# Optimization experiments

Measured on AMD Instinct MI355X. Metric: run time of the kernel, lower is better.

Reference implementation:

```python
import jax, jax.numpy as jnp
import numpy as np

# dims (see shape_source)
N = 100000          # num_ent
E = 400000          # num edges
B = 2048            # batch of (sub, rel) queries
INIT_DIM = 100
UFD = 100           # user_fe_dim
ENT_DIM = INIT_DIM + 3 * UFD   # feature_method='concat' -> 400
H = 2               # attention heads
D = 64              # per-head dim
GCN = H * D         # gcn_dim = embed_dim = 128 (gcn_layer == 1)
NUM_REL = 50
NR2 = 2 * NUM_REL


def setup_inputs() -> dict:
    key = jax.random.key(0)
    ks = jax.random.split(key, 17)
    inp = {}
    # constructor / forward int tensors
    inp["edge_index"] = jax.random.randint(ks[0], (2, E), 0, N, dtype=jnp.int32)
    inp["edge_type"] = jax.random.randint(ks[1], (E,), 0, NR2, dtype=jnp.int32)
    inp["edge_type_p"] = jax.random.randint(ks[2], (E,), 0, NR2, dtype=jnp.int32)
    inp["ent_feature"] = jax.random.randint(ks[3], (N, 3), 0, 3, dtype=jnp.int32)
    inp["sub"] = jax.random.randint(ks[4], (B,), 0, N, dtype=jnp.int32)
    inp["rel"] = jax.random.randint(ks[5], (B,), 0, NR2, dtype=jnp.int32)
    inp["relp"] = jax.random.randint(ks[6], (B,), 0, NR2, dtype=jnp.int32)
    # learned parameters
    s = 0.02
    inp["id_embed"] = jax.random.normal(ks[7], (N, INIT_DIM), jnp.float32) * s
    inp["gender_tab"] = jax.random.normal(ks[8], (3, UFD), jnp.float32) * s
    inp["age_tab"] = jax.random.normal(ks[9], (9, UFD), jnp.float32) * s
    inp["level_tab"] = jax.random.normal(ks[10], (11, UFD), jnp.float32) * s
    inp["init_rel"] = jax.random.normal(ks[11], (NR2, ENT_DIM), jnp.float32) * s
    inp["W"] = jax.random.normal(ks[12], (ENT_DIM, H * D), jnp.float32) * 0.05
    inp["Wr"] = jax.random.normal(ks[13], (ENT_DIM, H * D), jnp.float32) * 0.05
    inp["att_src"] = jax.random.normal(ks[14], (H, D), jnp.float32) * 0.05
    inp["att_dst"] = jax.random.normal(ks[15], (H, D), jnp.float32) * 0.05
    inp["Wrel"] = jax.random.normal(ks[16], (ENT_DIM, GCN), jnp.float32) * 0.05
    return inp


def _segment_softmax(logits, seg, num_segments):
    # logits: [E, H], seg: [E] destination node ids
    m = jax.ops.segment_max(logits, seg, num_segments=num_segments)
    ex = jnp.exp(logits - m[seg])
    den = jax.ops.segment_sum(ex, seg, num_segments=num_segments)
    return ex / (den[seg] + 1e-16)


def _rghat_conv(x, rel_emb, edge_index, edge_type, W, Wr, att_src, att_dst, Wrel):
    # relational multi-head graph attention (RGHATConv)
    n = x.shape[0]
    h = (x @ W).reshape(n, H, D)                       # [N,H,D] projected nodes
    r_proj = (rel_emb @ Wr).reshape(-1, H, D)          # [R,H,D]
    src, dst = edge_index[0], edge_index[1]
    msg = h[src] + r_proj[edge_type]                   # [E,H,D] edge messages
    logits = jax.nn.leaky_relu(
        jnp.sum(msg * att_src, axis=-1) + jnp.sum(h[dst] * att_dst, axis=-1),
        negative_slope=0.2,
    )                                                  # [E,H]
    alpha = _segment_softmax(logits, dst, n)           # per-destination softmax
    out = jax.ops.segment_sum(alpha[..., None] * msg, dst, num_segments=n)
    out = jnp.tanh(out.reshape(n, H * D))              # [N,GCN]
    r_out = rel_emb @ Wrel                             # [R,GCN]
    return out, r_out


def reference(edge_index, edge_type, edge_type_p, ent_feature, sub, rel, relp,
              id_embed, gender_tab, age_tab, level_tab, init_rel,
              W, Wr, att_src, att_dst, Wrel):
    # feature_method == 'concat': gather per-node feature embeddings and concat
    x1 = gender_tab[ent_feature[:, 0]]
    x2 = age_tab[ent_feature[:, 1]]
    x3 = level_tab[ent_feature[:, 2]]
    init_embed = jnp.concatenate([id_embed, x1, x2, x3], axis=1)  # [N, ENT_DIM]
    # single conv layer (gcn_layer == 1); dropouts are identity in eval
    x, r = _rghat_conv(init_embed, init_rel, edge_index, edge_type,
                       W, Wr, att_src, att_dst, Wrel)
    sub_emb = x[sub]                                   # index_select gather
    # add_parent_rel == False -> r returned whole (relp unused)
    return (sub_emb, r, x)
```

## Files before the change

### kernel.cpp

```cpp
#include <hip/hip_runtime.h>
#include <hip/hip_bf16.h>
#include <hip/hip_fp16.h>

#define N_NODES 100000
#define E_EDGES 400000
#define B_SUB 2048
#define INIT_DIM 100
#define UFD 100
#define ENT_DIM 400
#define GCN 128
#define NR2 100
#define KPAD 416
#define NCH 13
#define CAP 64

typedef __attribute__((ext_vector_type(8))) short shortx8;
typedef __attribute__((ext_vector_type(4))) float floatx4;

#define OUT_R_OFF ((long)B_SUB * GCN)
#define OUT_X_OFF ((long)(B_SUB + NR2) * GCN)

__device__ __forceinline__ unsigned short f2b(float f) {
    unsigned u = __float_as_uint(f);
    u += 0x7fffu + ((u >> 16) & 1u);
    return (unsigned short)(u >> 16);
}
__device__ __forceinline__ unsigned pk2(float x, float y) {
    return (unsigned)f2b(x) | ((unsigned)f2b(y) << 16);
}
__device__ __forceinline__ float blo(unsigned u) { return __uint_as_float(u << 16); }
__device__ __forceinline__ float bhi(unsigned u) { return __uint_as_float(u & 0xFFFF0000u); }

__global__ void wt_kernel(const float* __restrict__ W, unsigned short* __restrict__ Wt,
                          int* __restrict__ cursor) {
    int idx = blockIdx.x * 256 + threadIdx.x;
    if (idx < GCN * KPAD) {
        int n = idx & 127, k = idx >> 7;
        unsigned short o = 0;
        if (k < ENT_DIM) o = f2b(W[(long)k * GCN + n]);
        Wt[(long)n * KPAD + k] = o;
    }
    if (idx < N_NODES) cursor[idx] = 0;
}

__global__ void rel_kernel(const float* __restrict__ init_rel, const float* __restrict__ Wr,
                           const float* __restrict__ Wrel, const float* __restrict__ att_src,
                           unsigned* __restrict__ rp_b, float* __restrict__ rproj_att,
                           float* __restrict__ out_r) {
    int rel = blockIdx.x;
    int tx = threadIdx.x;
    __shared__ float rl[ENT_DIM];
    __shared__ float accbuf[128];
    for (int k = tx; k < ENT_DIM; k += 128) rl[k] = init_rel[(long)rel * ENT_DIM + k];
    __syncthreads();
    float acc1 = 0.f, acc2 = 0.f;
    for (int k = 0; k < ENT_DIM; ++k) {
        float v = rl[k];
        acc1 += v * Wr[(long)k * GCN + tx];
        acc2 += v * Wrel[(long)k * GCN + tx];
    }
    out_r[rel * GCN + tx] = acc2;
    accbuf[tx] = acc1;
    int head = tx >> 6, d = tx & 63;
    float v = acc1 * att_src[head * 64 + d];
    for (int off = 32; off > 0; off >>= 1) v += __shfl_down(v, off, 64);
    if (d == 0) rproj_att[rel * 2 + head] = v;
    __syncthreads();
    if (tx < 64) rp_b[rel * 64 + tx] = pk2(accbuf[tx], accbuf[tx + 64]);
}

__device__ __forceinline__ float4 load_seg(const float* __restrict__ id_embed,
                                           const float* __restrict__ gtab,
                                           const float* __restrict__ atab,
                                           const float* __restrict__ ltab,
                                           int n, int f0, int f1, int f2, int kg) {
    if (kg < 100)      return *(const float4*)&id_embed[(long)n * INIT_DIM + kg];
    else if (kg < 200) return *(const float4*)&gtab[f0 * UFD + kg - 100];
    else if (kg < 300) return *(const float4*)&atab[f1 * UFD + kg - 200];
    else if (kg < 400) return *(const float4*)&ltab[f2 * UFD + kg - 300];
    return make_float4(0.f, 0.f, 0.f, 0.f);
}

__global__ __launch_bounds__(256) void hgemm_kernel(
        const float* __restrict__ id_embed, const float* __restrict__ gtab,
        const float* __restrict__ atab, const float* __restrict__ ltab,
        const int* __restrict__ ent_feature, const unsigned short* __restrict__ Wt,
        const float* __restrict__ att_src, const float* __restrict__ att_dst,
        unsigned* __restrict__ h_b, float* __restrict__ hsrc_att, float* __restrict__ hdst_att) {
    __shared__ __align__(16) unsigned short As[64 * 40];
    __shared__ __align__(16) unsigned short Bs[128 * 40];
    __shared__ float attS[128], attD[128];
    int t = threadIdx.x;
    if (t < 128) { attS[t] = att_src[t]; attD[t] = att_dst[t]; }
    int n0 = blockIdx.x * 64;
    int row = t >> 2, seg = t & 3;
    int n = n0 + row;
    bool okn = n < N_NODES;
    int f0 = 0, f1 = 0, f2 = 0;
    if (okn) {
        f0 = ent_feature[n * 3];
        f1 = ent_feature[n * 3 + 1];
        f2 = ent_feature[n * 3 + 2];
    }
    int w = t >> 6, lane = t & 63, quad = lane >> 4, l16 = lane & 15;
    int nB0 = t >> 2,          k00 = (t & 3) * 8;
    int nB1 = (t + 256) >> 2,  k01 = (t & 3) * 8;

    floatx4 acc[8];
#pragma unroll
    for (int c = 0; c < 8; ++c) acc[c] = (floatx4){0.f, 0.f, 0.f, 0.f};

    float4 va = make_float4(0.f, 0.f, 0.f, 0.f), vb = va;
    if (okn) {
        va = load_seg(id_embed, gtab, atab, ltab, n, f0, f1, f2, seg * 8);
        vb = load_seg(id_embed, gtab, atab, ltab, n, f0, f1, f2, seg * 8 + 4);
    }
    shortx8 pb0 = *(const shortx8*)&Wt[(long)nB0 * KPAD + k00];
    shortx8 pb1 = *(const shortx8*)&Wt[(long)nB1 * KPAD + k01];

    for (int ch = 0; ch < NCH; ++ch) {
        uint4 u;
        u.x = pk2(va.x, va.y); u.y = pk2(va.z, va.w);
        u.z = pk2(vb.x, vb.y); u.w = pk2(vb.z, vb.w);
        __syncthreads();
        *(uint4*)&As[row * 40 + seg * 8] = u;
        *(shortx8*)&Bs[nB0 * 40 + k00] = pb0;
        *(shortx8*)&Bs[nB1 * 40 + k01] = pb1;
        if (ch + 1 < NCH) {
            int kg = (ch + 1) * 32 + seg * 8;
            if (okn) {
                va = load_seg(id_embed, gtab, atab, ltab, n, f0, f1, f2, kg);
                vb = load_seg(id_embed, gtab, atab, ltab, n, f0, f1, f2, kg + 4);
            }
            pb0 = *(const shortx8*)&Wt[(long)nB0 * KPAD + (ch + 1) * 32 + k00];
            pb1 = *(const shortx8*)&Wt[(long)nB1 * KPAD + (ch + 1) * 32 + k01];
        }
        __syncthreads();
        shortx8 a = *(shortx8*)&As[(w * 16 + l16) * 40 + quad * 8];
#pragma unroll
        for (int c = 0; c < 8; ++c) {
            shortx8 b = *(shortx8*)&Bs[(c * 16 + l16) * 40 + quad * 8];
            acc[c] = __builtin_amdgcn_mfma_f32_16x16x32_bf16(a, b, acc[c], 0, 0, 0);
        }
    }
    int baseRow = n0 + w * 16 + quad * 4;
#pragma unroll
    for (int i = 0; i < 4; ++i) {
        int node = baseRow + i;
        bool ok = node < N_NODES;
#pragma unroll
        for (int c = 0; c < 4; ++c)
            if (ok) h_b[(long)node * 64 + c * 16 + l16] = pk2(acc[c][i], acc[c + 4][i]);
        float s0 = 0.f, s1 = 0.f, d0 = 0.f, d1 = 0.f;
#pragma unroll
        for (int c = 0; c < 8; ++c) {
            float v = acc[c][i];
            float as_ = attS[c * 16 + l16], ad_ = attD[c * 16 + l16];
            if (c < 4) { s0 += v * as_; d0 += v * ad_; }
            else       { s1 += v * as_; d1 += v * ad_; }
        }
#pragma unroll
        for (int m = 1; m < 16; m <<= 1) {
            s0 += __shfl_xor(s0, m, 64);
            s1 += __shfl_xor(s1, m, 64);
            d0 += __shfl_xor(d0, m, 64);
            d1 += __shfl_xor(d1, m, 64);
        }
        if (ok && l16 == 0) {
            hsrc_att[node * 2] = s0; hsrc_att[node * 2 + 1] = s1;
            hdst_att[node * 2] = d0; hdst_att[node * 2 + 1] = d1;
        }
    }
}

__global__ void fill_kernel(const int* __restrict__ edge_index, const int* __restrict__ edge_type,
                            int* __restrict__ cursor,
                            const float2* __restrict__ hsrc2, const float2* __restrict__ rpa2,
                            const float2* __restrict__ hdst2,
                            uint2* __restrict__ ebuf) {
    int e = blockIdx.x * blockDim.x + threadIdx.x;
    if (e >= E_EDGES) return;
    int src = edge_index[e];
    int dst = edge_index[E_EDGES + e];
    int et = edge_type[e];
    float2 hs = hsrc2[src];
    float2 ra = rpa2[et];
    float2 hd = hdst2[dst];
    float x0 = hs.x + ra.x + hd.x;
    float x1 = hs.y + ra.y + hd.y;
    x0 = x0 > 0.f ? x0 : 0.2f * x0;
    x1 = x1 > 0.f ? x1 : 0.2f * x1;
    __half2 hh = __floats2half2_rn(__expf(x0), __expf(x1));
    union { __half2 h; unsigned u; } cv; cv.h = hh;
    int pos = atomicAdd(&cursor[dst], 1);
    if (pos < CAP)
        ebuf[(long)dst * CAP + pos] = make_uint2(((unsigned)et << 17) | (unsigned)src, cv.u);
}

__global__ __launch_bounds__(256) void agg_kernel(
        const int* __restrict__ cursor, const uint2* __restrict__ ebuf,
        const unsigned* __restrict__ h_b, const unsigned* __restrict__ rp_b,
        float* __restrict__ out_x) {
    int w = threadIdx.x >> 6, l = threadIdx.x & 63;
    int dst = blockIdx.x * 4 + w;
    int cnt = cursor[dst];
    if (cnt > CAP) cnt = CAP;
    const uint2* base = ebuf + (long)dst * CAP;
    float acc0 = 0.f, acc1 = 0.f, den0 = 0.f, den1 = 0.f;
    int j = 0;
    for (; j + 3 < cnt; j += 4) {
        uint2 v0 = base[j], v1 = base[j + 1], v2 = base[j + 2], v3 = base[j + 3];
        union { __half2 h; unsigned u; } c0, c1, c2, c3;
        c0.u = v0.y; c1.u = v1.y; c2.u = v2.y; c3.u = v3.y;
        float2 e0 = __half22float2(c0.h), e1 = __half22float2(c1.h);
        float2 e2 = __half22float2(c2.h), e3 = __half22float2(c3.h);
        unsigned hb0 = h_b[(long)(v0.x & 0x1FFFF) * 64 + l];
        unsigned hb1 = h_b[(long)(v1.x & 0x1FFFF) * 64 + l];
        unsigned hb2 = h_b[(long)(v2.x & 0x1FFFF) * 64 + l];
        unsigned hb3 = h_b[(long)(v3.x & 0x1FFFF) * 64 + l];
        unsigned rb0 = rp_b[(v0.x >> 17) * 64 + l];
        unsigned rb1 = rp_b[(v1.x >> 17) * 64 + l];
        unsigned rb2 = rp_b[(v2.x >> 17) * 64 + l];
        unsigned rb3 = rp_b[(v3.x >> 17) * 64 + l];
        acc0 += e0.x * (blo(hb0) + blo(rb0)) + e1.x * (blo(hb1) + blo(rb1))
              + e2.x * (blo(hb2) + blo(rb2)) + e3.x * (blo(hb3) + blo(rb3));
        acc1 += e0.y * (bhi(hb0) + bhi(rb0)) + e1.y * (bhi(hb1) + bhi(rb1))
              + e2.y * (bhi(hb2) + bhi(rb2)) + e3.y * (bhi(hb3) + bhi(rb3));
        den0 += e0.x + e1.x + e2.x + e3.x;
        den1 += e0.y + e1.y + e2.y + e3.y;
    }
    for (; j < cnt; ++j) {
        uint2 v0 = base[j];
        union { __half2 h; unsigned u; } c0; c0.u = v0.y;
        float2 e0 = __half22float2(c0.h);
        unsigned hb = h_b[(long)(v0.x & 0x1FFFF) * 64 + l];
        unsigned rb = rp_b[(v0.x >> 17) * 64 + l];
        acc0 += e0.x * (blo(hb) + blo(rb));
        acc1 += e0.y * (bhi(hb) + bhi(rb));
        den0 += e0.x;
        den1 += e0.y;
    }
    float i0 = 1.0f / (den0 + 1e-16f), i1 = 1.0f / (den1 + 1e-16f);
    out_x[(long)dst * GCN + l] = tanhf(acc0 * i0);
    out_x[(long)dst * GCN + 64 + l] = tanhf(acc1 * i1);
}

__global__ void gather_kernel(const int* __restrict__ sub, const float* __restrict__ out_x,
                              float* __restrict__ out_sub) {
    int idx = blockIdx.x * blockDim.x + threadIdx.x;
    if (idx >= B_SUB * GCN) return;
    int b = idx >> 7, d = idx & 127;
    out_sub[idx] = out_x[(long)sub[b] * GCN + d];
}

extern "C" void kernel_launch(void* const* d_in, const int* in_sizes, int n_in,
                              void* d_out, int out_size, void* d_ws, size_t ws_size,
                              hipStream_t stream) {
    const int* edge_index = (const int*)d_in[0];
    const int* edge_type  = (const int*)d_in[1];
    const int* ent_feature = (const int*)d_in[3];
    const int* sub = (const int*)d_in[4];
    const float* id_embed = (const float*)d_in[7];
    const float* gtab = (const float*)d_in[8];
    const float* atab = (const float*)d_in[9];
    const float* ltab = (const float*)d_in[10];
    const float* init_rel = (const float*)d_in[11];
    const float* W = (const float*)d_in[12];
    const float* Wr = (const float*)d_in[13];
    const float* att_src = (const float*)d_in[14];
    const float* att_dst = (const float*)d_in[15];
    const float* Wrel = (const float*)d_in[16];

    char* ws = (char*)d_ws;
    unsigned* h_b = (unsigned*)ws;                          ws += (long)N_NODES * 64 * 4;
    unsigned* rp_b = (unsigned*)ws;                         ws += (long)NR2 * 64 * 4;
    float* rproj_att = (float*)ws;                          ws += NR2 * 2 * 4;
    float* hsrc_att = (float*)ws;                           ws += (long)N_NODES * 2 * 4;
    float* hdst_att = (float*)ws;                           ws += (long)N_NODES * 2 * 4;
    unsigned short* Wt = (unsigned short*)ws;               ws += (long)GCN * KPAD * 2;
    int* cursor = (int*)ws;                                 ws += (long)N_NODES * 4;
    uint2* ebuf = (uint2*)ws;                               ws += (long)N_NODES * CAP * 8;

    float* out = (float*)d_out;
    float* out_sub = out;
    float* out_r = out + OUT_R_OFF;
    float* out_x = out + OUT_X_OFF;

    const int NB = (N_NODES + 255) / 256;

    wt_kernel<<<NB, 256, 0, stream>>>(W, Wt, cursor);
    rel_kernel<<<NR2, 128, 0, stream>>>(init_rel, Wr, Wrel, att_src, rp_b, rproj_att, out_r);
    hgemm_kernel<<<(N_NODES + 63) / 64, 256, 0, stream>>>(id_embed, gtab, atab, ltab,
                                                          ent_feature, Wt, att_src, att_dst,
                                                          h_b, hsrc_att, hdst_att);
    fill_kernel<<<(E_EDGES + 255) / 256, 256, 0, stream>>>(edge_index, edge_type, cursor,
                                                           (const float2*)hsrc_att,
                                                           (const float2*)rproj_att,
                                                           (const float2*)hdst_att, ebuf);
    agg_kernel<<<N_NODES / 4, 256, 0, stream>>>(cursor, ebuf, h_b, rp_b, out_x);
    gather_kernel<<<(B_SUB * GCN + 255) / 256, 256, 0, stream>>>(sub, out_x, out_sub);
}
```

Before: 242.8 us.

## Use direct global-to-LDS double-buffered loads in hgemm and split rel_kernel K

The node-projection GEMM now stages fp32 A tiles and bf16 B tiles straight into LDS with global_load_lds into double buffers using an XOR swizzle, and converts A to bf16 at fragment-read time with v_cvt_pk_bf16_f32. This takes register staging and the second barrier off each K chunk so global loads overlap with MFMA. The relation kernel splits K across two thread halves and sums the partials in shared memory, the attention vectors move into registers, and the aggregation output uses nontemporal stores. The new swizzled staging is more complex, and the loop is fully unrolled with per-row segment pointers, which raises register pressure.

```diff
diff --git a/kernel.cpp b/kernel.cpp
--- a/kernel.cpp
+++ b/kernel.cpp
@@ -12,6 +12,7 @@
 #define NR2 100
 #define KPAD 416
 #define NCH 13
+#define CHK 32
 #define CAP 64
 
 typedef __attribute__((ext_vector_type(8))) short shortx8;
@@ -27,6 +28,11 @@
 }
 __device__ __forceinline__ unsigned pk2(float x, float y) {
     return (unsigned)f2b(x) | ((unsigned)f2b(y) << 16);
+}
+__device__ __forceinline__ unsigned cvtpk2(float x, float y) {
+    unsigned r;
+    asm("v_cvt_pk_bf16_f32 %0, %1, %2" : "=v"(r) : "v"(x), "v"(y));
+    return r;
 }
 __device__ __forceinline__ float blo(unsigned u) { return __uint_as_float(u << 16); }
 __device__ __forceinline__ float bhi(unsigned u) { return __uint_as_float(u & 0xFFFF0000u); }
@@ -43,42 +49,46 @@
     if (idx < N_NODES) cursor[idx] = 0;
 }
 
-__global__ void rel_kernel(const float* __restrict__ init_rel, const float* __restrict__ Wr,
-                           const float* __restrict__ Wrel, const float* __restrict__ att_src,
-                           unsigned* __restrict__ rp_b, float* __restrict__ rproj_att,
-                           float* __restrict__ out_r) {
+__global__ __launch_bounds__(256) void rel_kernel(
+        const float* __restrict__ init_rel, const float* __restrict__ Wr,
+        const float* __restrict__ Wrel, const float* __restrict__ att_src,
+        unsigned* __restrict__ rp_b, float* __restrict__ rproj_att,
+        float* __restrict__ out_r) {
     int rel = blockIdx.x;
-    int tx = threadIdx.x;
+    int t = threadIdx.x;
+    int tx = t & 127, kh = t >> 7;
     __shared__ float rl[ENT_DIM];
+    __shared__ float p1[2][128], p2[2][128];
     __shared__ float accbuf[128];
-    for (int k = tx; k < ENT_DIM; k += 128) rl[k] = init_rel[(long)rel * ENT_DIM + k];
+    for (int k = t; k < ENT_DIM; k += 256) rl[k] = init_rel[(long)rel * ENT_DIM + k];
     __syncthreads();
-    float acc1 = 0.f, acc2 = 0.f;
-    for (int k = 0; k < ENT_DIM; ++k) {
-        float v = rl[k];
-        acc1 += v * Wr[(long)k * GCN + tx];
-        acc2 += v * Wrel[(long)k * GCN + tx];
-    }
-    out_r[rel * GCN + tx] = acc2;
-    accbuf[tx] = acc1;
-    int head = tx >> 6, d = tx & 63;
-    float v = acc1 * att_src[head * 64 + d];
-    for (int off = 32; off > 0; off >>= 1) v += __shfl_down(v, off, 64);
-    if (d == 0) rproj_att[rel * 2 + head] = v;
+    float a1 = 0.f, a2 = 0.f;
+    {
+        const float* wr = Wr + (long)(kh * 200) * GCN + tx;
+        const float* wl = Wrel + (long)(kh * 200) * GCN + tx;
+        const float* rv = rl + kh * 200;
+#pragma unroll 8
+        for (int k = 0; k < 200; ++k) {
+            float v = rv[k];
+            a1 += v * wr[(long)k * GCN];
+            a2 += v * wl[(long)k * GCN];
+        }
+    }
+    p1[kh][tx] = a1;
+    p2[kh][tx] = a2;
     __syncthreads();
-    if (tx < 64) rp_b[rel * 64 + tx] = pk2(accbuf[tx], accbuf[tx + 64]);
-}
-
-__device__ __forceinline__ float4 load_seg(const float* __restrict__ id_embed,
-                                           const float* __restrict__ gtab,
-                                           const float* __restrict__ atab,
-                                           const float* __restrict__ ltab,
-                                           int n, int f0, int f1, int f2, int kg) {
-    if (kg < 100)      return *(const float4*)&id_embed[(long)n * INIT_DIM + kg];
-    else if (kg < 200) return *(const float4*)&gtab[f0 * UFD + kg - 100];
-    else if (kg < 300) return *(const float4*)&atab[f1 * UFD + kg - 200];
-    else if (kg < 400) return *(const float4*)&ltab[f2 * UFD + kg - 300];
-    return make_float4(0.f, 0.f, 0.f, 0.f);
+    if (t < 128) {
+        float acc1 = p1[0][tx] + p1[1][tx];
+        float acc2 = p2[0][tx] + p2[1][tx];
+        out_r[rel * GCN + tx] = acc2;
+        accbuf[tx] = acc1;
+        int head = tx >> 6, d = tx & 63;
+        float v = acc1 * att_src[head * 64 + d];
+        for (int off = 32; off > 0; off >>= 1) v += __shfl_down(v, off, 64);
+        if (d == 0) rproj_att[rel * 2 + head] = v;
+    }
+    __syncthreads();
+    if (t < 64) rp_b[rel * 64 + t] = pk2(accbuf[t], accbuf[t + 64]);
 }
 
 __global__ __launch_bounds__(256) void hgemm_kernel(
@@ -87,61 +97,89 @@
         const int* __restrict__ ent_feature, const unsigned short* __restrict__ Wt,
         const float* __restrict__ att_src, const float* __restrict__ att_dst,
         unsigned* __restrict__ h_b, float* __restrict__ hsrc_att, float* __restrict__ hdst_att) {
-    __shared__ __align__(16) unsigned short As[64 * 40];
-    __shared__ __align__(16) unsigned short Bs[128 * 40];
-    __shared__ float attS[128], attD[128];
+    __shared__ __align__(16) float As[2][64 * CHK];
+    __shared__ __align__(16) unsigned short Bs[2][128 * CHK];
+
     int t = threadIdx.x;
-    if (t < 128) { attS[t] = att_src[t]; attD[t] = att_dst[t]; }
+    int w = t >> 6, lane = t & 63, quad = lane >> 4, l16 = lane & 15;
     int n0 = blockIdx.x * 64;
-    int row = t >> 2, seg = t & 3;
-    int n = n0 + row;
-    bool okn = n < N_NODES;
-    int f0 = 0, f1 = 0, f2 = 0;
-    if (okn) {
-        f0 = ent_feature[n * 3];
-        f1 = ent_feature[n * 3 + 1];
-        f2 = ent_feature[n * 3 + 2];
-    }
-    int w = t >> 6, lane = t & 63, quad = lane >> 4, l16 = lane & 15;
-    int nB0 = t >> 2,          k00 = (t & 3) * 8;
-    int nB1 = (t + 256) >> 2,  k01 = (t & 3) * 8;
+
+    int rA = t >> 3;
+    int lA4 = ((t & 7) ^ (rA & 7)) * 4;
+    const float* segp[2][4];
+#pragma unroll
+    for (int rr = 0; rr < 2; ++rr) {
+        int node = n0 + rr * 32 + rA;
+        int nc = node < N_NODES ? node : N_NODES - 1;
+        segp[rr][0] = id_embed + (long)nc * INIT_DIM;
+        segp[rr][1] = gtab + ent_feature[nc * 3] * UFD;
+        segp[rr][2] = atab + ent_feature[nc * 3 + 1] * UFD;
+        segp[rr][3] = ltab + ent_feature[nc * 3 + 2] * UFD;
+    }
+    int cB = t >> 2;
+    int lB8 = ((t & 3) ^ ((t >> 3) & 3)) * 8;
+    const unsigned short* bsrc0 = Wt + (long)cB * KPAD + lB8;
+    const unsigned short* bsrc1 = Wt + (long)(64 + cB) * KPAD + lB8;
+
+#define SEGPTR(rr_, kg_) ((kg_) < 100 ? segp[rr_][0] + (kg_) : \
+                          (kg_) < 200 ? segp[rr_][1] + ((kg_) - 100) : \
+                          (kg_) < 300 ? segp[rr_][2] + ((kg_) - 200) : \
+                          (kg_) < 400 ? segp[rr_][3] + ((kg_) - 300) : segp[rr_][0])
+
+#define STAGE(ch_, bi_) { \
+    int kgA_ = (ch_) * CHK + lA4; \
+    __builtin_amdgcn_global_load_lds( \
+        (const __attribute__((address_space(1))) unsigned*)SEGPTR(0, kgA_), \
+        (__attribute__((address_space(3))) unsigned*)((char*)&As[bi_][0] + w * 1024), 16, 0, 0); \
+    __builtin_amdgcn_global_load_lds( \
+        (const __attribute__((address_space(1))) unsigned*)SEGPTR(1, kgA_), \
+        (__attribute__((address_space(3))) unsigned*)((char*)&As[bi_][0] + 4096 + w * 1024), 16, 0, 0); \
+    __builtin_amdgcn_global_load_lds( \
+        (const __attribute__((address_space(1))) unsigned*)(bsrc0 + (ch_) * CHK), \
+        (__attribute__((address_space(3))) unsigned*)((char*)&Bs[bi_][0] + w * 1024), 16, 0, 0); \
+    __builtin_amdgcn_global_load_lds( \
+        (const __attribute__((address_space(1))) unsigned*)(bsrc1 + (ch_) * CHK), \
+        (__attribute__((address_space(3))) unsigned*)((char*)&Bs[bi_][0] + 4096 + w * 1024), 16, 0, 0); \
+}
 
     floatx4 acc[8];
 #pragma unroll
     for (int c = 0; c < 8; ++c) acc[c] = (floatx4){0.f, 0.f, 0.f, 0.f};
 
-    float4 va = make_float4(0.f, 0.f, 0.f, 0.f), vb = va;
-    if (okn) {
-        va = load_seg(id_embed, gtab, atab, ltab, n, f0, f1, f2, seg * 8);
-        vb = load_seg(id_embed, gtab, atab, ltab, n, f0, f1, f2, seg * 8 + 4);
-    }
-    shortx8 pb0 = *(const shortx8*)&Wt[(long)nB0 * KPAD + k00];
-    shortx8 pb1 = *(const shortx8*)&Wt[(long)nB1 * KPAD + k01];
-
+    int xA0 = (2 * quad) ^ (l16 & 7);
+    int xA1 = (2 * quad + 1) ^ (l16 & 7);
+    int qB = quad ^ ((l16 >> 1) & 3);
+
+#define COMPUTE(bi_) { \
+    const float* arow_ = &As[bi_][0] + (w * 16 + l16) * CHK; \
+    float4 fa0_ = *(const float4*)(arow_ + xA0 * 4); \
+    float4 fa1_ = *(const float4*)(arow_ + xA1 * 4); \
+    uint4 u_; \
+    u_.x = cvtpk2(fa0_.x, fa0_.y); u_.y = cvtpk2(fa0_.z, fa0_.w); \
+    u_.z = cvtpk2(fa1_.x, fa1_.y); u_.w = cvtpk2(fa1_.z, fa1_.w); \
+    shortx8 af_ = *(shortx8*)&u_; \
+    _Pragma("unroll") for (int c = 0; c < 8; ++c) { \
+        shortx8 b_ = *(const shortx8*)(&Bs[bi_][0] + (c * 16 + l16) * CHK + qB * 8); \
+        acc[c] = __builtin_amdgcn_mfma_f32_16x16x32_bf16(af_, b_, acc[c], 0, 0, 0); \
+    } \
+}
+
+    STAGE(0, 0);
+#pragma unroll
     for (int ch = 0; ch < NCH; ++ch) {
-        uint4 u;
-        u.x = pk2(va.x, va.y); u.y = pk2(va.z, va.w);
-        u.z = pk2(vb.x, vb.y); u.w = pk2(vb.z, vb.w);
         __syncthreads();
-        *(uint4*)&As[row * 40 + seg * 8] = u;
-        *(shortx8*)&Bs[nB0 * 40 + k00] = pb0;
-        *(shortx8*)&Bs[nB1 * 40 + k01] = pb1;
-        if (ch + 1 < NCH) {
-            int kg = (ch + 1) * 32 + seg * 8;
-            if (okn) {
-                va = load_seg(id_embed, gtab, atab, ltab, n, f0, f1, f2, kg);
-                vb = load_seg(id_embed, gtab, atab, ltab, n, f0, f1, f2, kg + 4);
-            }
-            pb0 = *(const shortx8*)&Wt[(long)nB0 * KPAD + (ch + 1) * 32 + k00];
-            pb1 = *(const shortx8*)&Wt[(long)nB1 * KPAD + (ch + 1) * 32 + k01];
-        }
-        __syncthreads();
-        shortx8 a = *(shortx8*)&As[(w * 16 + l16) * 40 + quad * 8];
-#pragma unroll
-        for (int c = 0; c < 8; ++c) {
-            shortx8 b = *(shortx8*)&Bs[(c * 16 + l16) * 40 + quad * 8];
-            acc[c] = __builtin_amdgcn_mfma_f32_16x16x32_bf16(a, b, acc[c], 0, 0, 0);
-        }
+        if (ch + 1 < NCH) STAGE(ch + 1, (ch & 1) ^ 1);
+        COMPUTE(ch & 1);
+    }
+#undef STAGE
+#undef COMPUTE
+#undef SEGPTR
+
+    float attS_r[8], attD_r[8];
+#pragma unroll
+    for (int c = 0; c < 8; ++c) {
+        attS_r[c] = att_src[c * 16 + l16];
+        attD_r[c] = att_dst[c * 16 + l16];
     }
     int baseRow = n0 + w * 16 + quad * 4;
 #pragma unroll
@@ -150,14 +188,13 @@
         bool ok = node < N_NODES;
 #pragma unroll
         for (int c = 0; c < 4; ++c)
-            if (ok) h_b[(long)node * 64 + c * 16 + l16] = pk2(acc[c][i], acc[c + 4][i]);
+            if (ok) h_b[(long)node * 64 + c * 16 + l16] = cvtpk2(acc[c][i], acc[c + 4][i]);
         float s0 = 0.f, s1 = 0.f, d0 = 0.f, d1 = 0.f;
 #pragma unroll
         for (int c = 0; c < 8; ++c) {
             float v = acc[c][i];
-            float as_ = attS[c * 16 + l16], ad_ = attD[c * 16 + l16];
-            if (c < 4) { s0 += v * as_; d0 += v * ad_; }
-            else       { s1 += v * as_; d1 += v * ad_; }
+            if (c < 4) { s0 += v * attS_r[c]; d0 += v * attD_r[c]; }
+            else       { s1 += v * attS_r[c]; d1 += v * attD_r[c]; }
         }
 #pragma unroll
         for (int m = 1; m < 16; m <<= 1) {
@@ -167,8 +204,8 @@
             d1 += __shfl_xor(d1, m, 64);
         }
         if (ok && l16 == 0) {
-            hsrc_att[node * 2] = s0; hsrc_att[node * 2 + 1] = s1;
-            hdst_att[node * 2] = d0; hdst_att[node * 2 + 1] = d1;
+            *(float2*)&hsrc_att[node * 2] = make_float2(s0, s1);
+            *(float2*)&hdst_att[node * 2] = make_float2(d0, d1);
         }
     }
 }
@@ -241,8 +278,8 @@
         den1 += e0.y;
     }
     float i0 = 1.0f / (den0 + 1e-16f), i1 = 1.0f / (den1 + 1e-16f);
-    out_x[(long)dst * GCN + l] = tanhf(acc0 * i0);
-    out_x[(long)dst * GCN + 64 + l] = tanhf(acc1 * i1);
+    __builtin_nontemporal_store(tanhf(acc0 * i0), &out_x[(long)dst * GCN + l]);
+    __builtin_nontemporal_store(tanhf(acc1 * i1), &out_x[(long)dst * GCN + 64 + l]);
 }
 
 __global__ void gather_kernel(const int* __restrict__ sub, const float* __restrict__ out_x,
@@ -289,7 +326,7 @@
     const int NB = (N_NODES + 255) / 256;
 
     wt_kernel<<<NB, 256, 0, stream>>>(W, Wt, cursor);
-    rel_kernel<<<NR2, 128, 0, stream>>>(init_rel, Wr, Wrel, att_src, rp_b, rproj_att, out_r);
+    rel_kernel<<<NR2, 256, 0, stream>>>(init_rel, Wr, Wrel, att_src, rp_b, rproj_att, out_r);
     hgemm_kernel<<<(N_NODES + 63) / 64, 256, 0, stream>>>(id_embed, gtab, atab, ltab,
                                                           ent_feature, Wt, att_src, att_dst,
                                                           h_b, hsrc_att, hdst_att);
```

Result: faster. 233.7 us (-3.8%).
